# Performance work log

Hardware: AMD Instinct MI355X
Metric: run time of the kernel (lower is better)

## Reference

```python
import jax, jax.numpy as jnp
import numpy as np

VOCAB, E, S, B = 50000, 256, 512, 4
E4 = 4 * E
ALPHA = 1.5


def spectral_filter(mag, alpha=ALPHA):
    # \u03a8QRH spectral filter: F(k) = exp(i*alpha*arctan(ln|k|)) in Fourier domain
    n = mag.shape[-1]
    k = jnp.abs(jnp.fft.fftfreq(n) * n)  # |k| indices
    filt = jnp.exp(1j * alpha * jnp.arctan(jnp.log(k + 1e-6)))
    F = jnp.fft.fft(mag.astype(jnp.complex64), axis=-1)
    return jnp.real(jnp.fft.ifft(F * filt, axis=-1)).astype(mag.dtype)


def safe_spectral_filter(x):
    # vectorized form of the per-(b,t) Python loop: |x| -> spectral filter -> re-sign
    return spectral_filter(jnp.abs(x)) * jnp.sign(x)


def layer_norm(x, g, b, eps=1e-5):
    mu = jnp.mean(x, axis=-1, keepdims=True)
    var = jnp.var(x, axis=-1, keepdims=True)
    return (x - mu) * jax.lax.rsqrt(var + eps) * g + b


def setup_inputs() -> dict:
    key = jax.random.key(0)
    ks = jax.random.split(key, 20)
    def lin(k, fan_in, fan_out):
        bound = 1.0 / np.sqrt(fan_in)
        kw, kb = jax.random.split(k)
        w = jax.random.uniform(kw, (fan_in, fan_out), jnp.float32, -bound, bound)
        b = jax.random.uniform(kb, (fan_out,), jnp.float32, -bound, bound)
        return w, b
    char_ids = jax.random.randint(ks[0], (B, S), 0, VOCAB)
    emb = jax.random.normal(ks[1], (VOCAB, E), jnp.float32)
    # language_decoder: Linear(4E,2E) GELU LN(2E) Linear(2E,E) GELU Linear(E,vocab)
    dw1, db1 = lin(ks[2], E4, 2 * E)
    ln_g = jnp.ones((2 * E,), jnp.float32)
    ln_b = jnp.zeros((2 * E,), jnp.float32)
    dw2, db2 = lin(ks[3], 2 * E, E)
    dw3, db3 = lin(ks[4], E, VOCAB)
    # concept_recognizer: Linear(4E,E) ReLU Linear(E,64) ReLU Linear(64,32)
    cw1, cb1 = lin(ks[5], E4, E)
    cw2, cb2 = lin(ks[6], E, 64)
    cw3, cb3 = lin(ks[7], 64, 32)
    # structure_generator: Linear(32,16) ReLU Linear(16,8) Sigmoid
    sw1, sb1 = lin(ks[8], 32, 16)
    sw2, sb2 = lin(ks[9], 16, 8)
    return dict(char_ids=char_ids, emb=emb,
                dw1=dw1, db1=db1, ln_g=ln_g, ln_b=ln_b,
                dw2=dw2, db2=db2, dw3=dw3, db3=db3,
                cw1=cw1, cb1=cb1, cw2=cw2, cb2=cb2, cw3=cw3, cb3=cb3,
                sw1=sw1, sb1=sb1, sw2=sw2, sb2=sb2)


def reference(char_ids, emb, dw1, db1, ln_g, ln_b, dw2, db2, dw3, db3,
              cw1, cb1, cw2, cb2, cw3, cb3, sw1, sb1, sw2, sb2):
    x = emb[char_ids]                       # [B,S,E]
    x4 = jnp.tile(x, (1, 1, 4))             # [B,S,4E] (x.repeat(1,1,4))
    # semantic / QRH / neurotransmitter stages fall through as identity (except path)
    x_spec = safe_spectral_filter(x4)       # [B,S,4E]
    # concept recognizer -> mean over seq
    c = jax.nn.relu(jnp.einsum('bsd,de->bse', x_spec, cw1) + cb1)
    c = jax.nn.relu(c @ cw2 + cb2)
    concept_vector = (c @ cw3 + cb3).mean(axis=1)          # [B,32]
    structure_probs = jax.nn.sigmoid(
        jax.nn.relu(concept_vector @ sw1 + sb1) @ sw2 + sb2)  # [B,8]
    # language decoder
    h = jax.nn.gelu(jnp.einsum('bsd,de->bse', x_spec, dw1) + db1, approximate=False)
    h = layer_norm(h, ln_g, ln_b)
    h = jax.nn.gelu(h @ dw2 + db2, approximate=False)
    logits = h @ dw3 + db3                  # [B,S,VOCAB]
    return logits, concept_vector, structure_probs
```

## Files before the change

### kernel.cpp

```cpp
#include <hip/hip_runtime.h>
#include <math.h>

#define NVOCAB 50000
#define NE 256
#define NS 512
#define NB 4
#define NT 2048

#define OFF_G     0
#define OFF_GMAT  256
#define OFF_CW1   (OFF_GMAT + 65536)
#define OFF_DW1   (OFF_CW1 + 65536)
#define OFF_XS    (OFF_DW1 + 131072)
#define OFF_H2    (OFF_XS + 524288)
#define OFF_CA    (OFF_H2 + 524288)
#define OFF_AH    (OFF_CA + 128)
#define OFF_AL    (OFF_AH + 262144)
#define OFF_BH    (OFF_AL + 262144)
#define OFF_BL    (OFF_BH + 6400000)
#define WS_TOTAL_F (OFF_BL + 6400000)

typedef short bf16x8 __attribute__((ext_vector_type(8)));
typedef float f32x4 __attribute__((ext_vector_type(4)));
typedef unsigned short us8 __attribute__((ext_vector_type(8)));

__device__ __forceinline__ float gelu_exact(float x) {
  return 0.5f * x * (1.0f + erff(x * 0.70710678118654752440f));
}

__device__ __forceinline__ unsigned short f2bf(float x) {
  unsigned u = __float_as_uint(x);
  u += 0x7FFFu + ((u >> 16) & 1u);
  return (unsigned short)(u >> 16);
}
__device__ __forceinline__ float bf2f(unsigned short h) {
  return __uint_as_float(((unsigned)h) << 16);
}

__global__ __launch_bounds__(256) void k_prep1(float* ws) {
  int t = threadIdx.x;
  if (blockIdx.x == 0) {
    float sum = 0.f;
    for (int m = 0; m < 256; m++) {
      int mm = (m <= 128) ? m : (256 - m);
      float c = cosf(1.5f * atanf(logf(4.0f * (float)mm + 1e-6f)));
      int r = (m * t) & 255;
      sum += c * cosf((float)r * (6.283185307179586f / 256.0f));
    }
    ws[OFF_G + t] = sum * (1.0f / 256.0f);
  } else {
    if (t < 128) ws[OFF_CA + t] = 0.0f;
  }
}

__global__ __launch_bounds__(256) void k_prep2(const float* cw1, const float* dw1, float* ws) {
  int b = blockIdx.x, t = threadIdx.x;
  if (b < 256) {
    int d = b;
    ws[OFF_GMAT + d * 256 + t] = ws[OFF_G + ((t - d) & 255)];
  } else if (b < 512) {
    int r = b - 256;
    float s = 0.f;
    #pragma unroll
    for (int q = 0; q < 4; q++) s += cw1[(q * 256 + r) * 256 + t];
    ws[OFF_CW1 + r * 256 + t] = s;
  } else {
    int idx = (b - 512) * 256 + t;
    int r = idx >> 9, c = idx & 511;
    float s = 0.f;
    #pragma unroll
    for (int q = 0; q < 4; q++) s += dw1[(q * 256 + r) * 512 + c];
    ws[OFF_DW1 + idx] = s;
  }
}

__global__ __launch_bounds__(256) void k_spectral(const int* ids, const float* emb, float* ws) {
  __shared__ __align__(16) float xb[8][256];
  int t = threadIdx.x;
  int i0 = blockIdx.x * 8;
  #pragma unroll
  for (int rr = 0; rr < 8; rr++) {
    int id = ids[i0 + rr];
    xb[rr][t] = emb[id * 256 + t];
  }
  __syncthreads();
  float acc[8] = {0, 0, 0, 0, 0, 0, 0, 0};
  const float* Gm = ws + OFF_GMAT;
  for (int d = 0; d < 256; d += 4) {
    float w0 = Gm[(d + 0) * 256 + t];
    float w1 = Gm[(d + 1) * 256 + t];
    float w2 = Gm[(d + 2) * 256 + t];
    float w3 = Gm[(d + 3) * 256 + t];
    #pragma unroll
    for (int rr = 0; rr < 8; rr++) {
      float4 a4 = *(const float4*)&xb[rr][d];
      acc[rr] += fabsf(a4.x) * w0 + fabsf(a4.y) * w1 + fabsf(a4.z) * w2 + fabsf(a4.w) * w3;
    }
  }
  #pragma unroll
  for (int rr = 0; rr < 8; rr++) {
    float x = xb[rr][t];
    float sg = (x > 0.f) ? 1.f : ((x < 0.f) ? -1.f : 0.f);
    ws[OFF_XS + (i0 + rr) * 256 + t] = acc[rr] * sg;
  }
}

__global__ __launch_bounds__(256) void k_concept(const float* cb1, const float* cw2, const float* cb2,
                                                 const float* cw3, const float* cb3, float* ws) {
  __shared__ __align__(16) float xs_s[8][256];
  __shared__ __align__(16) float c1s[8][256];
  __shared__ float c2s[8][64];
  __shared__ float c3s[8][32];
  int t = threadIdx.x;
  int i0 = blockIdx.x * 8;
  #pragma unroll
  for (int rr = 0; rr < 8; rr++) xs_s[rr][t] = ws[OFF_XS + (i0 + rr) * 256 + t];
  __syncthreads();
  const float* cw1eff = ws + OFF_CW1;
  float acc[8] = {0, 0, 0, 0, 0, 0, 0, 0};
  for (int d = 0; d < 256; d += 4) {
    float w0 = cw1eff[(d + 0) * 256 + t];
    float w1 = cw1eff[(d + 1) * 256 + t];
    float w2 = cw1eff[(d + 2) * 256 + t];
    float w3 = cw1eff[(d + 3) * 256 + t];
    #pragma unroll
    for (int rr = 0; rr < 8; rr++) {
      float4 a4 = *(const float4*)&xs_s[rr][d];
      acc[rr] += a4.x * w0 + a4.y * w1 + a4.z * w2 + a4.w * w3;
    }
  }
  float b1v = cb1[t];
  #pragma unroll
  for (int rr = 0; rr < 8; rr++) c1s[rr][t] = fmaxf(acc[rr] + b1v, 0.f);
  __syncthreads();
  {
    int e = t & 63, grp = t >> 6;
    float a0 = 0.f, a1 = 0.f;
    for (int d = 0; d < 256; d++) {
      float w = cw2[d * 64 + e];
      a0 += c1s[grp * 2 + 0][d] * w;
      a1 += c1s[grp * 2 + 1][d] * w;
    }
    float b2v = cb2[e];
    c2s[grp * 2 + 0][e] = fmaxf(a0 + b2v, 0.f);
    c2s[grp * 2 + 1][e] = fmaxf(a1 + b2v, 0.f);
  }
  __syncthreads();
  {
    int v = t & 31, grp = t >> 5;
    float a = 0.f;
    for (int d = 0; d < 64; d++) a += c2s[grp][d] * cw3[d * 32 + v];
    c3s[grp][v] = a + cb3[v];
  }
  __syncthreads();
  if (t < 32) {
    float s = 0.f;
    #pragma unroll
    for (int rr = 0; rr < 8; rr++) s += c3s[rr][t];
    int bb = i0 >> 9;
    atomicAdd(ws + OFF_CA + bb * 32 + t, s * (1.0f / 512.0f));
  }
}

__global__ __launch_bounds__(128) void k_structure(const float* sw1, const float* sb1,
                                                   const float* sw2, const float* sb2,
                                                   float* out, const float* ws) {
  __shared__ float cv[4][32];
  __shared__ float s1[4][16];
  int t = threadIdx.x;
  {
    int b = t >> 5, j = t & 31;
    float v = ws[OFF_CA + t];
    cv[b][j] = v;
    out[102400000 + t] = v;
  }
  __syncthreads();
  if (t < 64) {
    int b = t >> 4, e = t & 15;
    float a = sb1[e];
    for (int d = 0; d < 32; d++) a += cv[b][d] * sw1[d * 16 + e];
    s1[b][e] = fmaxf(a, 0.f);
  }
  __syncthreads();
  if (t < 32) {
    int b = t >> 3, e = t & 7;
    float a = sb2[e];
    for (int d = 0; d < 16; d++) a += s1[b][d] * sw2[d * 8 + e];
    out[102400128 + t] = 1.0f / (1.0f + expf(-a));
  }
}

__global__ __launch_bounds__(256) void k_decoder(const float* db1, const float* lng, const float* lnb,
                                                 const float* dw2, const float* db2, float* ws) {
  __shared__ __align__(16) float xs_s[8][256];
  __shared__ __align__(16) float h1s[8][512];
  __shared__ float mu_s[8], rs_s[8];
  int t = threadIdx.x;
  int i0 = blockIdx.x * 8;
  #pragma unroll
  for (int rr = 0; rr < 8; rr++) xs_s[rr][t] = ws[OFF_XS + (i0 + rr) * 256 + t];
  __syncthreads();
  const float* dw1eff = ws + OFF_DW1;
  float a1[8] = {0, 0, 0, 0, 0, 0, 0, 0};
  float a2[8] = {0, 0, 0, 0, 0, 0, 0, 0};
  for (int d = 0; d < 256; d += 2) {
    float wa0 = dw1eff[(d + 0) * 512 + t];
    float wb0 = dw1eff[(d + 0) * 512 + t + 256];
    float wa1 = dw1eff[(d + 1) * 512 + t];
    float wb1 = dw1eff[(d + 1) * 512 + t + 256];
    #pragma unroll
    for (int rr = 0; rr < 8; rr++) {
      float2 x2 = *(const float2*)&xs_s[rr][d];
      a1[rr] += x2.x * wa0 + x2.y * wa1;
      a2[rr] += x2.x * wb0 + x2.y * wb1;
    }
  }
  float ba = db1[t], bb = db1[t + 256];
  #pragma unroll
  for (int rr = 0; rr < 8; rr++) {
    h1s[rr][t]       = gelu_exact(a1[rr] + ba);
    h1s[rr][t + 256] = gelu_exact(a2[rr] + bb);
  }
  __syncthreads();
  {
    int rr = t >> 5, q = t & 31;
    float sum = 0.f, sq = 0.f;
    for (int j = q; j < 512; j += 32) {
      float v = h1s[rr][j];
      sum += v; sq += v * v;
    }
    #pragma unroll
    for (int off = 16; off >= 1; off >>= 1) {
      sum += __shfl_down(sum, off, 32);
      sq  += __shfl_down(sq, off, 32);
    }
    if (q == 0) {
      float mu = sum * (1.0f / 512.0f);
      float var = sq * (1.0f / 512.0f) - mu * mu;
      mu_s[rr] = mu;
      rs_s[rr] = rsqrtf(var + 1e-5f);
    }
  }
  __syncthreads();
  {
    float ga = lng[t], bba = lnb[t], gb = lng[t + 256], bbb = lnb[t + 256];
    #pragma unroll
    for (int rr = 0; rr < 8; rr++) {
      float m = mu_s[rr], r = rs_s[rr];
      h1s[rr][t]       = (h1s[rr][t]       - m) * r * ga + bba;
      h1s[rr][t + 256] = (h1s[rr][t + 256] - m) * r * gb + bbb;
    }
  }
  __syncthreads();
  float acc[8] = {0, 0, 0, 0, 0, 0, 0, 0};
  for (int d = 0; d < 512; d += 2) {
    float w0 = dw2[(d + 0) * 256 + t];
    float w1 = dw2[(d + 1) * 256 + t];
    #pragma unroll
    for (int rr = 0; rr < 8; rr++) {
      float2 h2v = *(const float2*)&h1s[rr][d];
      acc[rr] += h2v.x * w0 + h2v.y * w1;
    }
  }
  float b2v = db2[t];
  #pragma unroll
  for (int rr = 0; rr < 8; rr++)
    ws[OFF_H2 + (i0 + rr) * 256 + t] = gelu_exact(acc[rr] + b2v);
}

__global__ __launch_bounds__(256) void k_splitA(float* ws) {
  int idx = (blockIdx.x * 256 + threadIdx.x) * 8;
  const float* h2 = ws + OFF_H2;
  unsigned short* Ah = (unsigned short*)(ws + OFF_AH);
  unsigned short* Al = (unsigned short*)(ws + OFF_AL);
  float4 v0 = *(const float4*)&h2[idx];
  float4 v1 = *(const float4*)&h2[idx + 4];
  float v[8] = {v0.x, v0.y, v0.z, v0.w, v1.x, v1.y, v1.z, v1.w};
  us8 h, l;
  #pragma unroll
  for (int i = 0; i < 8; i++) {
    unsigned short hb = f2bf(v[i]);
    h[i] = (short)hb;
    l[i] = (short)f2bf(v[i] - bf2f(hb));
  }
  *(us8*)&Ah[idx] = h;
  *(us8*)&Al[idx] = l;
}

__global__ __launch_bounds__(256) void k_splitB(const float* dw3, float* ws) {
  __shared__ float tile[64][65];
  int t = threadIdx.x;
  int n0 = blockIdx.x * 64;
  int k0 = blockIdx.y * 64;
  int tc = t & 15, tr = t >> 4;
  #pragma unroll
  for (int p = 0; p < 4; p++) {
    int k = k0 + tr + p * 16;
    int n = n0 + tc * 4;
    float4 v = make_float4(0.f, 0.f, 0.f, 0.f);
    if (n < NVOCAB) v = *(const float4*)&dw3[(size_t)k * NVOCAB + n];
    tile[tr + p * 16][tc * 4 + 0] = v.x;
    tile[tr + p * 16][tc * 4 + 1] = v.y;
    tile[tr + p * 16][tc * 4 + 2] = v.z;
    tile[tr + p * 16][tc * 4 + 3] = v.w;
  }
  __syncthreads();
  int nl = t >> 2, kq = (t & 3) * 16;
  int n = n0 + nl;
  if (n < NVOCAB) {
    unsigned short* Bh = (unsigned short*)(ws + OFF_BH);
    unsigned short* Bl = (unsigned short*)(ws + OFF_BL);
    us8 h0, h1, l0, l1;
    #pragma unroll
    for (int i = 0; i < 8; i++) {
      float x = tile[kq + i][nl];
      unsigned short hb = f2bf(x);
      h0[i] = (short)hb;
      l0[i] = (short)f2bf(x - bf2f(hb));
    }
    #pragma unroll
    for (int i = 0; i < 8; i++) {
      float x = tile[kq + 8 + i][nl];
      unsigned short hb = f2bf(x);
      h1[i] = (short)hb;
      l1[i] = (short)f2bf(x - bf2f(hb));
    }
    size_t base = (size_t)n * 256 + k0 + kq;
    *(us8*)&Bh[base] = h0;
    *(us8*)&Bh[base + 8] = h1;
    *(us8*)&Bl[base] = l0;
    *(us8*)&Bl[base + 8] = l1;
  }
}

__global__ __launch_bounds__(256, 2) void k_logits_mfma(const float* db3, float* out, const float* ws) {
  __shared__ __align__(16) unsigned short As[128 * 64];
  __shared__ __align__(16) unsigned short Bs[128 * 64];
  const unsigned short* Ah = (const unsigned short*)(ws + OFF_AH);
  const unsigned short* Al = (const unsigned short*)(ws + OFF_AL);
  const unsigned short* Bh = (const unsigned short*)(ws + OFF_BH);
  const unsigned short* Bl = (const unsigned short*)(ws + OFF_BL);
  int t = threadIdx.x;
  int n0 = blockIdx.x * 128;
  int m0 = blockIdx.y * 128;
  int lane = t & 63;
  int w = t >> 6;
  int wm = w >> 1, wn = w & 1;
  int rr = lane & 15, g = lane >> 4;

  f32x4 acc[4][4];
  #pragma unroll
  for (int i = 0; i < 4; i++)
    #pragma unroll
    for (int j = 0; j < 4; j++)
      acc[i][j] = (f32x4){0.f, 0.f, 0.f, 0.f};

  const us8 zero8 = {0, 0, 0, 0, 0, 0, 0, 0};

  for (int kk = 0; kk < 8; kk++) {
    int k0 = kk * 32;
    us8 ga[4], gb[4];
    #pragma unroll
    for (int p = 0; p < 4; p++) {
      int q = t + p * 256;
      int row = q >> 3, slot = q & 7;
      int joct = slot & 3;
      const unsigned short* srcA = (slot < 4) ? Ah : Al;
      ga[p] = *(const us8*)&srcA[(size_t)(m0 + row) * 256 + k0 + joct * 8];
      int n = n0 + row;
      if (n < NVOCAB) {
        const unsigned short* srcB = (slot < 4) ? Bh : Bl;
        gb[p] = *(const us8*)&srcB[(size_t)n * 256 + k0 + joct * 8];
      } else {
        gb[p] = zero8;
      }
    }
    __syncthreads();
    #pragma unroll
    for (int p = 0; p < 4; p++) {
      int q = t + p * 256;
      int row = q >> 3, slot = q & 7;
      int st = ((slot ^ (row & 7)) << 3);
      *(us8*)&As[row * 64 + st] = ga[p];
      *(us8*)&Bs[row * 64 + st] = gb[p];
    }
    __syncthreads();
    bf16x8 fah[4], fal[4], fbh[4], fbl[4];
    #pragma unroll
    for (int i = 0; i < 4; i++) {
      int m = wm * 64 + i * 16 + rr;
      int base = m * 64, sw = m & 7;
      fah[i] = *(const bf16x8*)&As[base + ((g ^ sw) << 3)];
      fal[i] = *(const bf16x8*)&As[base + (((4 + g) ^ sw) << 3)];
    }
    #pragma unroll
    for (int j = 0; j < 4; j++) {
      int c = wn * 64 + j * 16 + rr;
      int base = c * 64, sw = c & 7;
      fbh[j] = *(const bf16x8*)&Bs[base + ((g ^ sw) << 3)];
      fbl[j] = *(const bf16x8*)&Bs[base + (((4 + g) ^ sw) << 3)];
    }
    #pragma unroll
    for (int i = 0; i < 4; i++)
      #pragma unroll
      for (int j = 0; j < 4; j++) {
        acc[i][j] = __builtin_amdgcn_mfma_f32_16x16x32_bf16(fah[i], fbh[j], acc[i][j], 0, 0, 0);
        acc[i][j] = __builtin_amdgcn_mfma_f32_16x16x32_bf16(fah[i], fbl[j], acc[i][j], 0, 0, 0);
        acc[i][j] = __builtin_amdgcn_mfma_f32_16x16x32_bf16(fal[i], fbh[j], acc[i][j], 0, 0, 0);
      }
  }
  #pragma unroll
  for (int j = 0; j < 4; j++) {
    int n = n0 + wn * 64 + j * 16 + rr;
    if (n < NVOCAB) {
      float bias = db3[n];
      #pragma unroll
      for (int i = 0; i < 4; i++) {
        int mb = m0 + wm * 64 + i * 16 + g * 4;
        #pragma unroll
        for (int q2 = 0; q2 < 4; q2++) {
          out[(size_t)(mb + q2) * NVOCAB + n] = acc[i][j][q2] + bias;
        }
      }
    }
  }
}

__global__ __launch_bounds__(256) void k_logits(const float* dw3, const float* db3,
                                                float* out, const float* ws) {
  __shared__ __align__(16) float Asl[16 * 128];
  __shared__ __align__(16) float Bsl[16 * 128];
  int t = threadIdx.x;
  int n0 = blockIdx.x * 128;
  int m0 = blockIdx.y * 128;
  int tx = t & 15, ty = t >> 4;
  const float* h2 = ws + OFF_H2;

  float acc[8][8];
  #pragma unroll
  for (int i = 0; i < 8; i++)
    #pragma unroll
    for (int j = 0; j < 8; j++) acc[i][j] = 0.f;

  int ar = t >> 1, ah = t & 1;
  int bk = t >> 4, bn = (t & 15) * 8;
  bool bval = (n0 + bn) < NVOCAB;

  for (int k0 = 0; k0 < 256; k0 += 16) {
    float4 av0 = *(const float4*)&h2[(m0 + ar) * 256 + k0 + ah * 8];
    float4 av1 = *(const float4*)&h2[(m0 + ar) * 256 + k0 + ah * 8 + 4];
    float4 bv0, bv1;
    if (bval) {
      const float* bp = dw3 + (size_t)(k0 + bk) * NVOCAB + n0 + bn;
      bv0 = *(const float4*)bp;
      bv1 = *(const float4*)(bp + 4);
    } else {
      bv0 = make_float4(0.f, 0.f, 0.f, 0.f);
      bv1 = make_float4(0.f, 0.f, 0.f, 0.f);
    }
    __syncthreads();
    {
      int kb = ah * 8;
      Asl[(kb + 0) * 128 + ar] = av0.x;
      Asl[(kb + 1) * 128 + ar] = av0.y;
      Asl[(kb + 2) * 128 + ar] = av0.z;
      Asl[(kb + 3) * 128 + ar] = av0.w;
      Asl[(kb + 4) * 128 + ar] = av1.x;
      Asl[(kb + 5) * 128 + ar] = av1.y;
      Asl[(kb + 6) * 128 + ar] = av1.z;
      Asl[(kb + 7) * 128 + ar] = av1.w;
      *(float4*)&Bsl[bk * 128 + bn] = bv0;
      *(float4*)&Bsl[bk * 128 + bn + 4] = bv1;
    }
    __syncthreads();
    #pragma unroll
    for (int k = 0; k < 16; k++) {
      float4 a0 = *(const float4*)&Asl[k * 128 + ty * 4];
      float4 a1 = *(const float4*)&Asl[k * 128 + 64 + ty * 4];
      float4 b0 = *(const float4*)&Bsl[k * 128 + tx * 4];
      float4 b1 = *(const float4*)&Bsl[k * 128 + 64 + tx * 4];
      float am[8] = {a0.x, a0.y, a0.z, a0.w, a1.x, a1.y, a1.z, a1.w};
      float bm[8] = {b0.x, b0.y, b0.z, b0.w, b1.x, b1.y, b1.z, b1.w};
      #pragma unroll
      for (int i = 0; i < 8; i++)
        #pragma unroll
        for (int j = 0; j < 8; j++)
          acc[i][j] += am[i] * bm[j];
    }
  }
  #pragma unroll
  for (int jj = 0; jj < 2; jj++) {
    int nb = n0 + jj * 64 + tx * 4;
    if (nb < NVOCAB) {
      float4 bias = *(const float4*)&db3[nb];
      #pragma unroll
      for (int i = 0; i < 8; i++) {
        int m = m0 + (i < 4 ? ty * 4 + i : 64 + ty * 4 + (i - 4));
        float4 o;
        o.x = acc[i][jj * 4 + 0] + bias.x;
        o.y = acc[i][jj * 4 + 1] + bias.y;
        o.z = acc[i][jj * 4 + 2] + bias.z;
        o.w = acc[i][jj * 4 + 3] + bias.w;
        *(float4*)&out[(size_t)m * NVOCAB + nb] = o;
      }
    }
  }
}

extern "C" void kernel_launch(void* const* d_in, const int* in_sizes, int n_in,
                              void* d_out, int out_size, void* d_ws, size_t ws_size,
                              hipStream_t stream) {
  const int*   ids = (const int*)d_in[0];
  const float* emb = (const float*)d_in[1];
  const float* dw1 = (const float*)d_in[2];
  const float* db1 = (const float*)d_in[3];
  const float* lng = (const float*)d_in[4];
  const float* lnb = (const float*)d_in[5];
  const float* dw2 = (const float*)d_in[6];
  const float* db2 = (const float*)d_in[7];
  const float* dw3 = (const float*)d_in[8];
  const float* db3 = (const float*)d_in[9];
  const float* cw1 = (const float*)d_in[10];
  const float* cb1 = (const float*)d_in[11];
  const float* cw2 = (const float*)d_in[12];
  const float* cb2 = (const float*)d_in[13];
  const float* cw3 = (const float*)d_in[14];
  const float* cb3 = (const float*)d_in[15];
  const float* sw1 = (const float*)d_in[16];
  const float* sb1 = (const float*)d_in[17];
  const float* sw2 = (const float*)d_in[18];
  const float* sb2 = (const float*)d_in[19];
  float* out = (float*)d_out;
  float* ws  = (float*)d_ws;

  bool mfma_ok = ws_size >= (size_t)WS_TOTAL_F * sizeof(float);

  hipLaunchKernelGGL(k_prep1, dim3(2), dim3(256), 0, stream, ws);
  hipLaunchKernelGGL(k_prep2, dim3(1024), dim3(256), 0, stream, cw1, dw1, ws);
  hipLaunchKernelGGL(k_spectral, dim3(256), dim3(256), 0, stream, ids, emb, ws);
  hipLaunchKernelGGL(k_concept, dim3(256), dim3(256), 0, stream, cb1, cw2, cb2, cw3, cb3, ws);
  hipLaunchKernelGGL(k_structure, dim3(1), dim3(128), 0, stream, sw1, sb1, sw2, sb2, out, ws);
  hipLaunchKernelGGL(k_decoder, dim3(256), dim3(256), 0, stream, db1, lng, lnb, dw2, db2, ws);
  if (mfma_ok) {
    hipLaunchKernelGGL(k_splitB, dim3(782, 4), dim3(256), 0, stream, dw3, ws);
    hipLaunchKernelGGL(k_splitA, dim3(256), dim3(256), 0, stream, ws);
    hipLaunchKernelGGL(k_logits_mfma, dim3(391, 16), dim3(256), 0, stream, db3, out, ws);
  } else {
    hipLaunchKernelGGL(k_logits, dim3(391, 16), dim3(256), 0, stream, dw3, db3, out, ws);
  }
}
```

Baseline: 883.1 us.

## Double-buffer logits MFMA tiles, swizzle block order, fuse A split into decoder

```diff
diff --git a/kernel.cpp b/kernel.cpp
--- a/kernel.cpp
+++ b/kernel.cpp
@@ -191,7 +191,8 @@
 }
 
 __global__ __launch_bounds__(256) void k_decoder(const float* db1, const float* lng, const float* lnb,
-                                                 const float* dw2, const float* db2, float* ws) {
+                                                 const float* dw2, const float* db2, float* ws,
+                                                 int emit_split) {
   __shared__ __align__(16) float xs_s[8][256];
   __shared__ __align__(16) float h1s[8][512];
   __shared__ float mu_s[8], rs_s[8];
@@ -263,28 +264,18 @@
     }
   }
   float b2v = db2[t];
-  #pragma unroll
-  for (int rr = 0; rr < 8; rr++)
-    ws[OFF_H2 + (i0 + rr) * 256 + t] = gelu_exact(acc[rr] + b2v);
-}
-
-__global__ __launch_bounds__(256) void k_splitA(float* ws) {
-  int idx = (blockIdx.x * 256 + threadIdx.x) * 8;
-  const float* h2 = ws + OFF_H2;
-  unsigned short* Ah = (unsigned short*)(ws + OFF_AH);
-  unsigned short* Al = (unsigned short*)(ws + OFF_AL);
-  float4 v0 = *(const float4*)&h2[idx];
-  float4 v1 = *(const float4*)&h2[idx + 4];
-  float v[8] = {v0.x, v0.y, v0.z, v0.w, v1.x, v1.y, v1.z, v1.w};
-  us8 h, l;
-  #pragma unroll
-  for (int i = 0; i < 8; i++) {
-    unsigned short hb = f2bf(v[i]);
-    h[i] = (short)hb;
-    l[i] = (short)f2bf(v[i] - bf2f(hb));
-  }
-  *(us8*)&Ah[idx] = h;
-  *(us8*)&Al[idx] = l;
+  unsigned short* Ahp = (unsigned short*)(ws + OFF_AH);
+  unsigned short* Alp = (unsigned short*)(ws + OFF_AL);
+  #pragma unroll
+  for (int rr = 0; rr < 8; rr++) {
+    float v = gelu_exact(acc[rr] + b2v);
+    ws[OFF_H2 + (i0 + rr) * 256 + t] = v;
+    if (emit_split) {
+      unsigned short hb = f2bf(v);
+      Ahp[(i0 + rr) * 256 + t] = hb;
+      Alp[(i0 + rr) * 256 + t] = f2bf(v - bf2f(hb));
+    }
+  }
 }
 
 __global__ __launch_bounds__(256) void k_splitB(const float* dw3, float* ws) {
@@ -334,15 +325,17 @@
 }
 
 __global__ __launch_bounds__(256, 2) void k_logits_mfma(const float* db3, float* out, const float* ws) {
-  __shared__ __align__(16) unsigned short As[128 * 64];
-  __shared__ __align__(16) unsigned short Bs[128 * 64];
+  __shared__ __align__(16) unsigned short As[2][128 * 64];
+  __shared__ __align__(16) unsigned short Bs[2][128 * 64];
   const unsigned short* Ah = (const unsigned short*)(ws + OFF_AH);
   const unsigned short* Al = (const unsigned short*)(ws + OFF_AL);
   const unsigned short* Bh = (const unsigned short*)(ws + OFF_BH);
   const unsigned short* Bl = (const unsigned short*)(ws + OFF_BL);
   int t = threadIdx.x;
-  int n0 = blockIdx.x * 128;
-  int m0 = blockIdx.y * 128;
+  int bid = blockIdx.x;
+  int work = ((bid & 7) * 782) + (bid >> 3);
+  int m0 = (work & 15) << 7;
+  int n0 = (work >> 4) << 7;
   int lane = t & 63;
   int w = t >> 6;
   int wm = w >> 1, wn = w & 1;
@@ -356,10 +349,10 @@
       acc[i][j] = (f32x4){0.f, 0.f, 0.f, 0.f};
 
   const us8 zero8 = {0, 0, 0, 0, 0, 0, 0, 0};
-
-  for (int kk = 0; kk < 8; kk++) {
+  us8 ga[4], gb[4];
+
+  auto LOADT = [&](int kk) {
     int k0 = kk * 32;
-    us8 ga[4], gb[4];
     #pragma unroll
     for (int p = 0; p < 4; p++) {
       int q = t + p * 256;
@@ -375,52 +368,66 @@
         gb[p] = zero8;
       }
     }
-    __syncthreads();
+  };
+  auto STORET = [&](int b) {
     #pragma unroll
     for (int p = 0; p < 4; p++) {
       int q = t + p * 256;
       int row = q >> 3, slot = q & 7;
       int st = ((slot ^ (row & 7)) << 3);
-      *(us8*)&As[row * 64 + st] = ga[p];
-      *(us8*)&Bs[row * 64 + st] = gb[p];
-    }
-    __syncthreads();
+      *(us8*)&As[b][row * 64 + st] = ga[p];
+      *(us8*)&Bs[b][row * 64 + st] = gb[p];
+    }
+  };
+
+  LOADT(0);
+  STORET(0);
+  __syncthreads();
+
+  #pragma unroll 2
+  for (int kk = 0; kk < 8; kk++) {
+    if (kk < 7) LOADT(kk + 1);
+    const unsigned short* Ab = As[kk & 1];
+    const unsigned short* Bb = Bs[kk & 1];
     bf16x8 fah[4], fal[4], fbh[4], fbl[4];
     #pragma unroll
     for (int i = 0; i < 4; i++) {
       int m = wm * 64 + i * 16 + rr;
       int base = m * 64, sw = m & 7;
-      fah[i] = *(const bf16x8*)&As[base + ((g ^ sw) << 3)];
-      fal[i] = *(const bf16x8*)&As[base + (((4 + g) ^ sw) << 3)];
+      fah[i] = *(const bf16x8*)&Ab[base + ((g ^ sw) << 3)];
+      fal[i] = *(const bf16x8*)&Ab[base + (((4 + g) ^ sw) << 3)];
     }
     #pragma unroll
     for (int j = 0; j < 4; j++) {
       int c = wn * 64 + j * 16 + rr;
       int base = c * 64, sw = c & 7;
-      fbh[j] = *(const bf16x8*)&Bs[base + ((g ^ sw) << 3)];
-      fbl[j] = *(const bf16x8*)&Bs[base + (((4 + g) ^ sw) << 3)];
+      fbh[j] = *(const bf16x8*)&Bb[base + ((g ^ sw) << 3)];
+      fbl[j] = *(const bf16x8*)&Bb[base + (((4 + g) ^ sw) << 3)];
     }
     #pragma unroll
     for (int i = 0; i < 4; i++)
       #pragma unroll
       for (int j = 0; j < 4; j++) {
-        acc[i][j] = __builtin_amdgcn_mfma_f32_16x16x32_bf16(fah[i], fbh[j], acc[i][j], 0, 0, 0);
-        acc[i][j] = __builtin_amdgcn_mfma_f32_16x16x32_bf16(fah[i], fbl[j], acc[i][j], 0, 0, 0);
-        acc[i][j] = __builtin_amdgcn_mfma_f32_16x16x32_bf16(fal[i], fbh[j], acc[i][j], 0, 0, 0);
+        acc[i][j] = __builtin_amdgcn_mfma_f32_16x16x32_bf16(fbh[j], fah[i], acc[i][j], 0, 0, 0);
+        acc[i][j] = __builtin_amdgcn_mfma_f32_16x16x32_bf16(fbl[j], fah[i], acc[i][j], 0, 0, 0);
+        acc[i][j] = __builtin_amdgcn_mfma_f32_16x16x32_bf16(fbh[j], fal[i], acc[i][j], 0, 0, 0);
       }
-  }
-  #pragma unroll
-  for (int j = 0; j < 4; j++) {
-    int n = n0 + wn * 64 + j * 16 + rr;
-    if (n < NVOCAB) {
-      float bias = db3[n];
-      #pragma unroll
-      for (int i = 0; i < 4; i++) {
-        int mb = m0 + wm * 64 + i * 16 + g * 4;
-        #pragma unroll
-        for (int q2 = 0; q2 < 4; q2++) {
-          out[(size_t)(mb + q2) * NVOCAB + n] = acc[i][j][q2] + bias;
-        }
+    if (kk < 7) {
+      STORET((kk + 1) & 1);
+      __syncthreads();
+    }
+  }
+
+  #pragma unroll
+  for (int i = 0; i < 4; i++) {
+    int m = m0 + wm * 64 + i * 16 + rr;
+    #pragma unroll
+    for (int j = 0; j < 4; j++) {
+      int nb = n0 + wn * 64 + j * 16 + g * 4;
+      if (nb < NVOCAB) {
+        f32x4 bias = *(const f32x4*)&db3[nb];
+        f32x4 o = acc[i][j] + bias;
+        __builtin_nontemporal_store(o, (f32x4*)(out + (size_t)m * NVOCAB + nb));
       }
     }
   }
@@ -537,14 +544,14 @@
 
   hipLaunchKernelGGL(k_prep1, dim3(2), dim3(256), 0, stream, ws);
   hipLaunchKernelGGL(k_prep2, dim3(1024), dim3(256), 0, stream, cw1, dw1, ws);
+  if (mfma_ok) hipLaunchKernelGGL(k_splitB, dim3(782, 4), dim3(256), 0, stream, dw3, ws);
   hipLaunchKernelGGL(k_spectral, dim3(256), dim3(256), 0, stream, ids, emb, ws);
   hipLaunchKernelGGL(k_concept, dim3(256), dim3(256), 0, stream, cb1, cw2, cb2, cw3, cb3, ws);
   hipLaunchKernelGGL(k_structure, dim3(1), dim3(128), 0, stream, sw1, sb1, sw2, sb2, out, ws);
-  hipLaunchKernelGGL(k_decoder, dim3(256), dim3(256), 0, stream, db1, lng, lnb, dw2, db2, ws);
+  hipLaunchKernelGGL(k_decoder, dim3(256), dim3(256), 0, stream, db1, lng, lnb, dw2, db2, ws,
+                     mfma_ok ? 1 : 0);
   if (mfma_ok) {
-    hipLaunchKernelGGL(k_splitB, dim3(782, 4), dim3(256), 0, stream, dw3, ws);
-    hipLaunchKernelGGL(k_splitA, dim3(256), dim3(256), 0, stream, ws);
-    hipLaunchKernelGGL(k_logits_mfma, dim3(391, 16), dim3(256), 0, stream, db3, out, ws);
+    hipLaunchKernelGGL(k_logits_mfma, dim3(6256), dim3(256), 0, stream, db3, out, ws);
   } else {
     hipLaunchKernelGGL(k_logits, dim3(391, 16), dim3(256), 0, stream, dw3, db3, out, ws);
   }
```

Measured after the change: 864.3 us. -2.1%, faster.
